# Optimization experiments

Measured on AMD Instinct MI355X. Metric: run time of the kernel, lower is better.

## Reference

```python
import jax, jax.numpy as jnp
import numpy as np

B, SW, SE, D, H, FF = 8, 512, 128, 1024, 16, 4096
HD = D // H
EPS = 1e-12
SCALE = 1.0 / np.sqrt(HD).astype(np.float32)


def _split_heads(x):
    # [B, S, D] -> [B, H, S, HD]
    b, s, _ = x.shape
    return x.reshape(b, s, H, HD).transpose(0, 2, 1, 3)


def _layer_norm(x, g, b):
    m = jnp.mean(x, axis=-1, keepdims=True)
    v = jnp.mean(jnp.square(x - m), axis=-1, keepdims=True)
    return g * (x - m) / jnp.sqrt(v + EPS) + b


def setup_inputs() -> dict:
    key = jax.random.key(0)
    ks = iter(jax.random.split(key, 40))
    std = 0.02

    def w(i, o):
        return jax.random.normal(next(ks), (i, o), jnp.float32) * std

    inp = {
        "word_hidden_states": jax.random.normal(next(ks), (B, SW, D), jnp.float32),
        "entity_hidden_states": jax.random.normal(next(ks), (B, SE, D), jnp.float32),
        "word_attention_mask": jnp.zeros((B, SW), jnp.float32),
        "entity_attention_mask": jnp.zeros((B, SE), jnp.float32),
        # entity-aware self attention projections
        "Wq": w(D, D), "bq": jnp.zeros((D,), jnp.float32),
        "Ww2e": w(D, D), "bw2e": jnp.zeros((D,), jnp.float32),
        "We2w": w(D, D), "be2w": jnp.zeros((D,), jnp.float32),
        "We2e": w(D, D), "be2e": jnp.zeros((D,), jnp.float32),
        "Wk": w(D, D), "bk": jnp.zeros((D,), jnp.float32),
        "Wv": w(D, D), "bv": jnp.zeros((D,), jnp.float32),
        # BertSelfOutput
        "Wo": w(D, D), "bo": jnp.zeros((D,), jnp.float32),
        "ln1_g": jnp.ones((D,), jnp.float32), "ln1_b": jnp.zeros((D,), jnp.float32),
        # BertIntermediate / BertOutput
        "Wi": w(D, FF), "bi": jnp.zeros((FF,), jnp.float32),
        "Wout": w(FF, D), "bout": jnp.zeros((D,), jnp.float32),
        "ln2_g": jnp.ones((D,), jnp.float32), "ln2_b": jnp.zeros((D,), jnp.float32),
    }
    return inp


def _layer(wh, eh, wmask, emask, Wq, bq, Ww2e, bw2e, We2w, be2w, We2e, be2e,
           Wk, bk, Wv, bv, Wo, bo, ln1_g, ln1_b, Wi, bi, Wout, bout, ln2_g, ln2_b):
    sw = wh.shape[1]
    hidden = jnp.concatenate([wh, eh], axis=1)              # [B, S, D]
    mask = jnp.concatenate([wmask, emask], axis=-1)[:, None, None, :]  # additive

    q_w2w = _split_heads(wh @ Wq + bq)
    q_w2e = _split_heads(wh @ Ww2e + bw2e)
    q_e2w = _split_heads(eh @ We2w + be2w)
    q_e2e = _split_heads(eh @ We2e + be2e)
    k = _split_heads(hidden @ Wk + bk)                      # [B, H, S, HD]
    kw, ke = k[:, :, :sw, :], k[:, :, sw:, :]

    s_w2w = jnp.einsum("bhqd,bhkd->bhqk", q_w2w, kw)
    s_w2e = jnp.einsum("bhqd,bhkd->bhqk", q_w2e, ke)
    s_e2w = jnp.einsum("bhqd,bhkd->bhqk", q_e2w, kw)
    s_e2e = jnp.einsum("bhqd,bhkd->bhqk", q_e2e, ke)
    word_scores = jnp.concatenate([s_w2w, s_w2e], axis=3)
    ent_scores = jnp.concatenate([s_e2w, s_e2e], axis=3)
    scores = jnp.concatenate([word_scores, ent_scores], axis=2) * SCALE + mask
    probs = jax.nn.softmax(scores, axis=-1)

    v = _split_heads(hidden @ Wv + bv)
    ctx = jnp.einsum("bhqk,bhkd->bhqd", probs, v)
    ctx = ctx.transpose(0, 2, 1, 3).reshape(wh.shape[0], -1, D)  # [B, S, D]

    # BertSelfOutput: dense + residual + LN
    attn_out = _layer_norm(ctx @ Wo + bo + hidden, ln1_g, ln1_b)
    # BertIntermediate + BertOutput
    inter = jax.nn.gelu(attn_out @ Wi + bi, approximate=False)
    out = _layer_norm(inter @ Wout + bout + attn_out, ln2_g, ln2_b)
    return out[:, :sw, :], out[:, sw:, :]


def reference(word_hidden_states, entity_hidden_states, word_attention_mask,
              entity_attention_mask, Wq, bq, Ww2e, bw2e, We2w, be2w, We2e, be2e,
              Wk, bk, Wv, bv, Wo, bo, ln1_g, ln1_b, Wi, bi, Wout, bout,
              ln2_g, ln2_b):
    return _layer(word_hidden_states, entity_hidden_states, word_attention_mask,
                  entity_attention_mask, Wq, bq, Ww2e, bw2e, We2w, be2w, We2e,
                  be2e, Wk, bk, Wv, bv, Wo, bo, ln1_g, ln1_b, Wi, bi, Wout,
                  bout, ln2_g, ln2_b)
```

## Files before the change

### kernel.cpp

```cpp
#include <hip/hip_runtime.h>
#include <hip/hip_bf16.h>
#include <stdint.h>
#include <math.h>

#define DEV __device__ __forceinline__

using bf16 = __hip_bfloat16;
typedef __attribute__((ext_vector_type(8))) short bf16x8;
typedef __attribute__((ext_vector_type(4))) float f32x4;

static constexpr int NB  = 8;
static constexpr int NSW = 512;
static constexpr int NSE = 128;
static constexpr int ND  = 1024;
static constexpr int NH  = 16;
static constexpr int NFF = 4096;
static constexpr int NS  = NSW + NSE;
static constexpr int NHD = 64;

DEV f32x4 mfma16(bf16x8 a, bf16x8 b, f32x4 c){
  return __builtin_amdgcn_mfma_f32_16x16x32_bf16(a, b, c, 0, 0, 0);
}

DEV void gload16(const bf16* g, bf16* l){
  __builtin_amdgcn_global_load_lds((const __attribute__((address_space(1))) void*)g,
                                   (__attribute__((address_space(3))) void*)l,
                                   16, 0, 0);
}

DEV bf16 tobf(float f){ return __float2bfloat16(f); }

union PK4 { bf16 h[4]; short4 s; };

__global__ __launch_bounds__(256) void cast_word_k(const float* __restrict__ wh,
                                                   bf16* __restrict__ hid){
  long i = ((long)blockIdx.x*256 + threadIdx.x)*4;
  float4 v = *reinterpret_cast<const float4*>(wh + i);
  PK4 p; p.h[0]=tobf(v.x); p.h[1]=tobf(v.y); p.h[2]=tobf(v.z); p.h[3]=tobf(v.w);
  long row = i >> 10; int c = (int)(i & 1023);
  int b = (int)(row >> 9), s = (int)(row & 511);
  *reinterpret_cast<short4*>(hid + ((long)(b*NS + s) << 10) + c) = p.s;
}

__global__ __launch_bounds__(256) void cast_ent_k(const float* __restrict__ eh,
                                                  bf16* __restrict__ hid){
  long i = ((long)blockIdx.x*256 + threadIdx.x)*4;
  float4 v = *reinterpret_cast<const float4*>(eh + i);
  PK4 p; p.h[0]=tobf(v.x); p.h[1]=tobf(v.y); p.h[2]=tobf(v.z); p.h[3]=tobf(v.w);
  long row = i >> 10; int c = (int)(i & 1023);
  int b = (int)(row >> 7), s = (int)(row & 127);
  *reinterpret_cast<short4*>(hid + ((long)(b*NS + NSW + s) << 10) + c) = p.s;
}

struct TP7 { const float* src[7]; bf16* dst[7]; };

__global__ void transpose7_k(TP7 tp){
  __shared__ float tile[32][33];
  const float* in = tp.src[blockIdx.z];
  bf16* out = tp.dst[blockIdx.z];
  const int c0 = blockIdx.x*32, r0 = blockIdx.y*32;
  const int tx = threadIdx.x, ty = threadIdx.y;
  #pragma unroll
  for (int i=0;i<4;i++)
    tile[ty + i*8][tx] = in[(long)(r0 + ty + i*8)*1024 + c0 + tx];
  __syncthreads();
  #pragma unroll
  for (int i=0;i<4;i++){
    int rr = ty + i*8;
    out[(long)(c0 + rr)*1024 + r0 + tx] = tobf(tile[tx][rr]);
  }
}

__global__ void transpose_cast_k(const float* __restrict__ in, bf16* __restrict__ out,
                                 int R, int C){
  __shared__ float tile[32][33];
  const int c0 = blockIdx.x*32, r0 = blockIdx.y*32;
  const int tx = threadIdx.x, ty = threadIdx.y;
  #pragma unroll
  for (int i=0;i<4;i++)
    tile[ty + i*8][tx] = in[(long)(r0 + ty + i*8)*C + c0 + tx];
  __syncthreads();
  #pragma unroll
  for (int i=0;i<4;i++){
    int rr = ty + i*8;
    out[(long)(c0 + rr)*R + r0 + tx] = tobf(tile[tx][rr]);
  }
}

__global__ void bias_concat_k(const float* __restrict__ bq, const float* __restrict__ bw2e,
                              const float* __restrict__ be2w, const float* __restrict__ be2e,
                              const float* __restrict__ bk, const float* __restrict__ bv,
                              float* __restrict__ bQw, float* __restrict__ bQe,
                              float* __restrict__ bKV){
  int i = blockIdx.x*256 + threadIdx.x;
  bQw[i] = bq[i];   bQw[1024+i] = bw2e[i];
  bQe[i] = be2w[i]; bQe[1024+i] = be2e[i];
  bKV[i] = bk[i];   bKV[1024+i] = bv[i];
}

template<int NF>
DEV void stage_issue(bf16* buf, const bf16* a0, const bf16* a1,
                     const bf16* b0, const bf16* b1, int koff, int tid){
  gload16(a0 + koff, buf + tid*8);
  gload16(a1 + koff, buf + (512 + tid)*8);
  gload16(b0 + koff, buf + (1024 + tid)*8);
  if constexpr (NF == 4) gload16(b1 + koff, buf + (1536 + tid)*8);
}

template<int NF>
DEV void g256_core(const bf16* a0, const bf16* a1,
                   const bf16* b0, const bf16* b1,
                   int NSs, bf16* lds, f32x4 (&acc)[8][NF],
                   int tid, int wr, int wc, int lane){
  constexpr int BUFE = (1024 + NF*256)*8;
  constexpr int LPS  = (NF == 4) ? 4 : 3;
  auto buf = [&](int s){ return lds + (s & 3)*BUFE; };

  stage_issue<NF>(buf(0), a0,a1,b0,b1, 0,  tid);
  stage_issue<NF>(buf(1), a0,a1,b0,b1, 32, tid);
  stage_issue<NF>(buf(2), a0,a1,b0,b1, 64, tid);

  for (int s=0; s<NSs; ++s){
    const int r = NSs - 1 - s;
    const int pend = (r >= 2 ? 2 : r) * LPS;
    if      (pend == 8) asm volatile("s_waitcnt vmcnt(8)" ::: "memory");
    else if (pend == 6) asm volatile("s_waitcnt vmcnt(6)" ::: "memory");
    else if (pend == 4) asm volatile("s_waitcnt vmcnt(4)" ::: "memory");
    else if (pend == 3) asm volatile("s_waitcnt vmcnt(3)" ::: "memory");
    else                asm volatile("s_waitcnt vmcnt(0)" ::: "memory");
    __builtin_amdgcn_sched_barrier(0);
    asm volatile("s_barrier" ::: "memory");
    __builtin_amdgcn_sched_barrier(0);

    if (s+3 < NSs) stage_issue<NF>(buf(s+3), a0,a1,b0,b1, (s+3)*32, tid);

    const bf16* Ar = buf(s);
    const bf16* Br = buf(s) + 1024*8;
    bf16x8 bfr[NF], afr[4];
    #pragma unroll
    for (int nf=0; nf<NF; ++nf)
      bfr[nf] = *reinterpret_cast<const bf16x8*>(Br + (((wc*NF+nf)<<6) + lane)*8);
    #pragma unroll
    for (int m=0; m<4; ++m)
      afr[m] = *reinterpret_cast<const bf16x8*>(Ar + (((wr*8+m)<<6) + lane)*8);
    __builtin_amdgcn_s_setprio(1);
    #pragma unroll
    for (int m=0; m<4; ++m)
      #pragma unroll
      for (int nf=0; nf<NF; ++nf)
        acc[m][nf] = mfma16(afr[m], bfr[nf], acc[m][nf]);
    __builtin_amdgcn_s_setprio(0);
    #pragma unroll
    for (int m=0; m<4; ++m)
      afr[m] = *reinterpret_cast<const bf16x8*>(Ar + (((wr*8+4+m)<<6) + lane)*8);
    __builtin_amdgcn_s_setprio(1);
    #pragma unroll
    for (int m=0; m<4; ++m)
      #pragma unroll
      for (int nf=0; nf<NF; ++nf)
        acc[4+m][nf] = mfma16(afr[m], bfr[nf], acc[4+m][nf]);
    __builtin_amdgcn_s_setprio(0);
  }
}

__global__ __launch_bounds__(512, 2) void proj_k(const bf16* __restrict__ hid,
    const bf16* __restrict__ WqwT, const bf16* __restrict__ WqeT,
    const bf16* __restrict__ WkvT,
    const float* __restrict__ bQw, const float* __restrict__ bQe,
    const float* __restrict__ bKV,
    bf16* __restrict__ Qwb, bf16* __restrict__ Qeb,
    bf16* __restrict__ KVb, bf16* __restrict__ Vt){
  __shared__ __align__(16) bf16 lds[4*16384];
  const int tid = threadIdx.x, wid = tid>>6, lane = tid&63;
  const int wr = wid>>2, wc = wid&3, lr = lane&15, lg = lane>>4;
  int wg = blockIdx.x;
  { int xcd = wg & 7, idx = wg >> 3; wg = xcd*40 + idx; }
  const bool isKV = (wg >= 160);
  const int loc = isKV ? wg - 160 : wg;
  const int m0 = (loc >> 3)*256, n0 = (loc & 7)*256;
  const bool word = (m0 < 4096);

  const int la = lane & 15, ksub = (lane>>4)*8;
  auto hidrow = [&](int r)->long{
    if (isKV) return r;
    if (word) return (long)((r>>9)*640 + (r&511));
    int r2 = r - 4096; return (long)((r2>>7)*640 + 512 + (r2&127));
  };
  const bf16* a0 = hid + hidrow(m0 + wid*16 + la)*1024 + ksub;
  const bf16* a1 = hid + hidrow(m0 + (wid+8)*16 + la)*1024 + ksub;
  const bf16* Bt = isKV ? WkvT : (word ? WqwT : WqeT);
  const bf16* b0 = Bt + (long)(n0 + wid*16 + la)*1024 + ksub;
  const bf16* b1 = Bt + (long)(n0 + (wid+8)*16 + la)*1024 + ksub;

  f32x4 acc[8][4];
  #pragma unroll
  for (int m=0;m<8;m++)
    #pragma unroll
    for (int n=0;n<4;n++) acc[m][n] = (f32x4){0.f,0.f,0.f,0.f};

  g256_core<4>(a0, a1, b0, b1, 32, lds, acc, tid, wr, wc, lane);

  const float* bias = isKV ? bKV : (word ? bQw : bQe);
  #pragma unroll
  for (int m=0;m<8;m++){
    const int rbase = m0 + wr*128 + m*16 + lg*4;
    #pragma unroll
    for (int nf=0;nf<4;nf++){
      const int col = n0 + wc*64 + nf*16 + lr;
      const float bsv = bias[col];
      #pragma unroll
      for (int r=0;r<4;r++){
        const int rw = rbase + r;
        const float v = acc[m][nf][r] + bsv;
        if (!isKV){
          if (word) Qwb[(long)rw*2048 + col] = tobf(v);
          else      Qeb[(long)(rw-4096)*2048 + col] = tobf(v);
        } else {
          if (col < 1024){
            KVb[(long)rw*2048 + col] = tobf(v);
          } else {
            int b = rw / NS, s = rw % NS, hh = (col-1024)>>6, dd = (col-1024)&63;
            Vt[((long)((b*NH + hh)*NHD + dd))*NS + s] = tobf(v);
          }
        }
      }
    }
  }
}

__global__ __launch_bounds__(512, 2) void ffn1_k(const bf16* __restrict__ A,
    const bf16* __restrict__ Bt, const float* __restrict__ bias,
    bf16* __restrict__ out){
  __shared__ __align__(16) bf16 lds[4*16384];
  const int tid = threadIdx.x, wid = tid>>6, lane = tid&63;
  const int wr = wid>>2, wc = wid&3, lr = lane&15, lg = lane>>4;
  int wg = blockIdx.x;
  { int xcd = wg & 7, idx = wg >> 3; wg = xcd*40 + idx; }
  const int m0 = (wg >> 4)*256, n0 = (wg & 15)*256;

  const int la = lane & 15, ksub = (lane>>4)*8;
  const bf16* a0 = A + (long)(m0 + wid*16 + la)*1024 + ksub;
  const bf16* a1 = A + (long)(m0 + (wid+8)*16 + la)*1024 + ksub;
  const bf16* b0 = Bt + (long)(n0 + wid*16 + la)*1024 + ksub;
  const bf16* b1 = Bt + (long)(n0 + (wid+8)*16 + la)*1024 + ksub;

  f32x4 acc[8][4];
  #pragma unroll
  for (int m=0;m<8;m++)
    #pragma unroll
    for (int n=0;n<4;n++) acc[m][n] = (f32x4){0.f,0.f,0.f,0.f};

  g256_core<4>(a0, a1, b0, b1, 32, lds, acc, tid, wr, wc, lane);

  #pragma unroll
  for (int m=0;m<8;m++){
    const int rbase = m0 + wr*128 + m*16 + lg*4;
    #pragma unroll
    for (int nf=0;nf<4;nf++){
      const int col = n0 + wc*64 + nf*16 + lr;
      const float bsv = bias[col];
      #pragma unroll
      for (int r=0;r<4;r++){
        float v = acc[m][nf][r] + bsv;
        float ge = 0.5f*v*(1.0f + erff(v*0.70710678118654752f));
        out[(long)(rbase+r)*NFF + col] = tobf(ge);
      }
    }
  }
}

__global__ __launch_bounds__(512, 2) void ws_k(const bf16* __restrict__ A, int lda,
    const bf16* __restrict__ Bt, const float* __restrict__ bias,
    float* __restrict__ out0, float* __restrict__ out1, int Kc){
  __shared__ __align__(16) bf16 lds[4*12288];
  const int tid = threadIdx.x, wid = tid>>6, lane = tid&63;
  const int wr = wid>>2, wc = wid&3, lr = lane&15, lg = lane>>4;
  int wg = blockIdx.x;
  { int xcd = wg & 7, idx = wg >> 3; wg = xcd*20 + idx; }
  const int m0 = (wg >> 3)*256, n0 = (wg & 7)*128;
  const int kt0 = blockIdx.z * Kc;

  const int la = lane & 15, ksub = (lane>>4)*8;
  const bf16* a0 = A + (long)(m0 + wid*16 + la)*lda + kt0 + ksub;
  const bf16* a1 = A + (long)(m0 + (wid+8)*16 + la)*lda + kt0 + ksub;
  const bf16* b0 = Bt + (long)(n0 + wid*16 + la)*lda + kt0 + ksub;

  f32x4 acc[8][2];
  #pragma unroll
  for (int m=0;m<8;m++)
    #pragma unroll
    for (int n=0;n<2;n++) acc[m][n] = (f32x4){0.f,0.f,0.f,0.f};

  g256_core<2>(a0, a1, b0, b0, Kc/32, lds, acc, tid, wr, wc, lane);

  float* out = blockIdx.z ? out1 : out0;
  #pragma unroll
  for (int m=0;m<8;m++){
    const int rbase = m0 + wr*128 + m*16 + lg*4;
    #pragma unroll
    for (int nf=0;nf<2;nf++){
      const int col = n0 + wc*32 + nf*16 + lr;
      const float bsv = blockIdx.z ? 0.f : bias[col];
      #pragma unroll
      for (int r=0;r<4;r++)
        out[(long)(rbase+r)*1024 + col] = acc[m][nf][r] + bsv;
    }
  }
}

__global__ __launch_bounds__(256) void attn_k(
    const bf16* __restrict__ Qw, const bf16* __restrict__ Qe,
    const bf16* __restrict__ KV, const bf16* __restrict__ Vt,
    const float* __restrict__ wm, const float* __restrict__ em,
    bf16* __restrict__ ctx){
  __shared__ __align__(16) bf16 Plds[4][2][16*40];
  __shared__ float mred[4][2][16];
  __shared__ float lred[4][2][16];
  __shared__ __align__(16) float accred[4][16][64];
  const int tid = threadIdx.x, wid = tid>>6, lane = tid&63;
  const int lr = lane&15, lg = lane>>4;
  const int w   = blockIdx.x;
  const int b   = w / (NH*20);
  const int rem = w % (NH*20);
  const int h   = rem / 20;
  const int q0  = (rem % 20)*32;

  const bf16* Qbase; long qrow0;
  if (q0 < NSW){ Qbase = Qw; qrow0 = (long)b*NSW + q0; }
  else         { Qbase = Qe; qrow0 = (long)b*NSE + (q0 - NSW); }

  bf16x8 qA[2][2], qB[2][2];
  #pragma unroll
  for (int m=0;m<2;m++)
    #pragma unroll
    for (int dc=0; dc<2; dc++){
      long o = (qrow0 + m*16 + lr)*2048 + h*NHD + dc*32 + lg*8;
      qA[m][dc] = *reinterpret_cast<const bf16x8*>(Qbase + o);
      qB[m][dc] = *reinterpret_cast<const bf16x8*>(Qbase + o + 1024);
    }

  const f32x4 zero = {0.f,0.f,0.f,0.f};
  f32x4 cacc[2][4];
  float mrow[2][4], lsum[2][4];
  #pragma unroll
  for (int m=0;m<2;m++){
    #pragma unroll
    for (int dt=0;dt<4;dt++) cacc[m][dt] = zero;
    #pragma unroll
    for (int r=0;r<4;r++){ mrow[m][r] = -1e30f; lsum[m][r] = 0.f; }
  }

  const bf16* Kbase = KV + (long)b*NS*2048 + h*NHD;
  const bf16* Vbase = Vt + (long)((b*NH + h)*NHD)*NS;

  for (int kt=wid*5; kt<wid*5+5; kt++){
    const int k0 = kt*32;
    const bool word = (k0 < NSW);

    bf16x8 kf[2][2], vf[4];
    #pragma unroll
    for (int sub=0;sub<2;sub++)
      #pragma unroll
      for (int dc=0;dc<2;dc++)
        kf[sub][dc] = *reinterpret_cast<const bf16x8*>(
            Kbase + (long)(k0 + sub*16 + lr)*2048 + dc*32 + lg*8);
    #pragma unroll
    for (int dt=0;dt<4;dt++)
      vf[dt] = *reinterpret_cast<const bf16x8*>(
          Vbase + (long)(dt*16 + lr)*NS + k0 + lg*8);

    float msk0, msk1;
    { int k = k0 + lr;
      msk0 = word ? wm[b*NSW + k]      : em[b*NSE + (k - NSW)];
      msk1 = word ? wm[b*NSW + k + 16] : em[b*NSE + (k + 16 - NSW)];
    }

    f32x4 sc[2][2];
    #pragma unroll
    for (int m=0;m<2;m++){ sc[m][0]=zero; sc[m][1]=zero; }
    __builtin_amdgcn_s_setprio(1);
    #pragma unroll
    for (int m=0;m<2;m++)
      #pragma unroll
      for (int sub=0;sub<2;sub++)
        #pragma unroll
        for (int dc=0;dc<2;dc++){
          const bf16x8 q = word ? qA[m][dc] : qB[m][dc];
          sc[m][sub] = mfma16(q, kf[sub][dc], sc[m][sub]);
        }
    __builtin_amdgcn_s_setprio(0);

    #pragma unroll
    for (int m=0;m<2;m++){
      bf16* pw = &Plds[wid][m][0];
      #pragma unroll
      for (int r=0;r<4;r++){
        float s0 = sc[m][0][r]*0.125f + msk0;
        float s1 = sc[m][1][r]*0.125f + msk1;
        float t = fmaxf(s0, s1);
        #pragma unroll
        for (int o=8;o;o>>=1) t = fmaxf(t, __shfl_xor(t, o, 16));
        float mn = fmaxf(mrow[m][r], t);
        float al = __expf(mrow[m][r] - mn);
        mrow[m][r] = mn;
        float p0 = __expf(s0 - mn), p1 = __expf(s1 - mn);
        float ps = p0 + p1;
        #pragma unroll
        for (int o=8;o;o>>=1) ps += __shfl_xor(ps, o, 16);
        lsum[m][r] = lsum[m][r]*al + ps;
        pw[(lg*4+r)*40 + lr]      = tobf(p0);
        pw[(lg*4+r)*40 + 16 + lr] = tobf(p1);
        #pragma unroll
        for (int dt=0;dt<4;dt++) cacc[m][dt][r] *= al;
      }
    }

    __builtin_amdgcn_s_setprio(1);
    #pragma unroll
    for (int m=0;m<2;m++){
      bf16x8 pa = *reinterpret_cast<const bf16x8*>(&Plds[wid][m][0] + lr*40 + lg*8);
      #pragma unroll
      for (int dt=0;dt<4;dt++)
        cacc[m][dt] = mfma16(pa, vf[dt], cacc[m][dt]);
    }
    __builtin_amdgcn_s_setprio(0);
  }

  #pragma unroll
  for (int m=0;m<2;m++)
    #pragma unroll
    for (int r=0;r<4;r++)
      if (lr == 0){
        mred[wid][m][lg*4+r] = mrow[m][r];
        lred[wid][m][lg*4+r] = lsum[m][r];
      }
  __syncthreads();

  float Lg[2][4], scl[2][4];
  #pragma unroll
  for (int m=0;m<2;m++)
    #pragma unroll
    for (int r=0;r<4;r++){
      const int row = lg*4 + r;
      float M0 = fmaxf(fmaxf(mred[0][m][row], mred[1][m][row]),
                       fmaxf(mred[2][m][row], mred[3][m][row]));
      float lt = 0.f;
      #pragma unroll
      for (int ww=0; ww<4; ww++)
        lt += lred[ww][m][row] * __expf(mred[ww][m][row] - M0);
      Lg[m][r]  = lt;
      scl[m][r] = __expf(mrow[m][r] - M0);
    }

  const long crow = (long)b*NS + q0;
  #pragma unroll
  for (int m=0;m<2;m++){
    #pragma unroll
    for (int dt=0;dt<4;dt++)
      #pragma unroll
      for (int r=0;r<4;r++)
        accred[wid][dt*4+r][lane] = cacc[m][dt][r] * scl[m][r];
    __syncthreads();
    { const int dt = wid;
      #pragma unroll
      for (int r=0;r<4;r++){
        float s = accred[0][dt*4+r][lane] + accred[1][dt*4+r][lane]
                + accred[2][dt*4+r][lane] + accred[3][dt*4+r][lane];
        s /= Lg[m][r];
        ctx[(crow + m*16 + lg*4 + r)*ND + h*NHD + dt*16 + lr] = tobf(s);
      }
    }
    __syncthreads();
  }
}

DEV void block_red2(float& s1, float& s2){
  __shared__ float red[8];
  #pragma unroll
  for (int o=32;o;o>>=1){ s1 += __shfl_down(s1,o); s2 += __shfl_down(s2,o); }
  int wid = threadIdx.x>>6, lane = threadIdx.x&63;
  if (lane==0){ red[wid]=s1; red[4+wid]=s2; }
  __syncthreads();
  s1 = red[0]+red[1]+red[2]+red[3];
  s2 = red[4]+red[5]+red[6]+red[7];
}

__global__ __launch_bounds__(256) void ln1_k(const float* __restrict__ ctxO,
    const float* __restrict__ ctxO1,
    const float* __restrict__ wh, const float* __restrict__ eh,
    const float* __restrict__ g, const float* __restrict__ be,
    float* __restrict__ outF, bf16* __restrict__ outB){
  const int row = blockIdx.x;
  const int b = row / NS, s = row % NS;
  const float* resid = (s < NSW) ? wh + ((long)(b*NSW + s))*ND
                                 : eh + ((long)(b*NSE + (s-NSW)))*ND;
  const int t = threadIdx.x;
  float4 xv = reinterpret_cast<const float4*>(ctxO + (long)row*ND)[t];
  float4 x1 = reinterpret_cast<const float4*>(ctxO1 + (long)row*ND)[t];
  float4 rv = reinterpret_cast<const float4*>(resid)[t];
  float4 x = make_float4(xv.x+x1.x+rv.x, xv.y+x1.y+rv.y, xv.z+x1.z+rv.z, xv.w+x1.w+rv.w);
  float s1 = x.x+x.y+x.z+x.w;
  float s2 = x.x*x.x + x.y*x.y + x.z*x.z + x.w*x.w;
  block_red2(s1, s2);
  float mean = s1 * (1.f/ND);
  float var  = s2 * (1.f/ND) - mean*mean;
  float rstd = rsqrtf(var + 1e-12f);
  float4 gv = reinterpret_cast<const float4*>(g)[t];
  float4 bv = reinterpret_cast<const float4*>(be)[t];
  float4 y = make_float4(gv.x*(x.x-mean)*rstd + bv.x,
                         gv.y*(x.y-mean)*rstd + bv.y,
                         gv.z*(x.z-mean)*rstd + bv.z,
                         gv.w*(x.w-mean)*rstd + bv.w);
  reinterpret_cast<float4*>(outF + (long)row*ND)[t] = y;
  PK4 p; p.h[0]=tobf(y.x); p.h[1]=tobf(y.y); p.h[2]=tobf(y.z); p.h[3]=tobf(y.w);
  reinterpret_cast<short4*>(outB + (long)row*ND)[t] = p.s;
}

__global__ __launch_bounds__(256) void ln2_k(const float* __restrict__ ffo,
    const float* __restrict__ ffo1,
    const float* __restrict__ attnF, const float* __restrict__ g,
    const float* __restrict__ be, float* __restrict__ out){
  const int row = blockIdx.x;
  const int b = row / NS, s = row % NS;
  const int t = threadIdx.x;
  float4 xv = reinterpret_cast<const float4*>(ffo + (long)row*ND)[t];
  float4 x1 = reinterpret_cast<const float4*>(ffo1 + (long)row*ND)[t];
  float4 rv = reinterpret_cast<const float4*>(attnF + (long)row*ND)[t];
  float4 x = make_float4(xv.x+x1.x+rv.x, xv.y+x1.y+rv.y, xv.z+x1.z+rv.z, xv.w+x1.w+rv.w);
  float s1 = x.x+x.y+x.z+x.w;
  float s2 = x.x*x.x + x.y*x.y + x.z*x.z + x.w*x.w;
  block_red2(s1, s2);
  float mean = s1 * (1.f/ND);
  float var  = s2 * (1.f/ND) - mean*mean;
  float rstd = rsqrtf(var + 1e-12f);
  float4 gv = reinterpret_cast<const float4*>(g)[t];
  float4 bv = reinterpret_cast<const float4*>(be)[t];
  float4 y = make_float4(gv.x*(x.x-mean)*rstd + bv.x,
                         gv.y*(x.y-mean)*rstd + bv.y,
                         gv.z*(x.z-mean)*rstd + bv.z,
                         gv.w*(x.w-mean)*rstd + bv.w);
  float* op = (s < NSW) ? out + ((long)(b*NSW+s))*ND
                        : out + (long)NB*NSW*ND + ((long)(b*NSE + (s-NSW)))*ND;
  reinterpret_cast<float4*>(op)[t] = y;
}

extern "C" void kernel_launch(void* const* d_in, const int* in_sizes, int n_in,
                              void* d_out, int out_size, void* d_ws, size_t ws_size,
                              hipStream_t stream){
  (void)in_sizes; (void)n_in; (void)out_size; (void)ws_size;
  const float* wh   = (const float*)d_in[0];
  const float* eh   = (const float*)d_in[1];
  const float* wm   = (const float*)d_in[2];
  const float* em   = (const float*)d_in[3];
  const float* Wq   = (const float*)d_in[4];   const float* bq   = (const float*)d_in[5];
  const float* Ww2e = (const float*)d_in[6];   const float* bw2e = (const float*)d_in[7];
  const float* We2w = (const float*)d_in[8];   const float* be2w = (const float*)d_in[9];
  const float* We2e = (const float*)d_in[10];  const float* be2e = (const float*)d_in[11];
  const float* Wk   = (const float*)d_in[12];  const float* bk   = (const float*)d_in[13];
  const float* Wv   = (const float*)d_in[14];  const float* bv   = (const float*)d_in[15];
  const float* Wo   = (const float*)d_in[16];  const float* bo   = (const float*)d_in[17];
  const float* g1   = (const float*)d_in[18];  const float* b1   = (const float*)d_in[19];
  const float* Wi   = (const float*)d_in[20];  const float* bi   = (const float*)d_in[21];
  const float* Wout = (const float*)d_in[22];  const float* bout = (const float*)d_in[23];
  const float* g2   = (const float*)d_in[24];  const float* b2   = (const float*)d_in[25];
  float* out = (float*)d_out;

  char* ws = (char*)d_ws;
  size_t off = 0;
  auto alloc = [&](size_t bytes)->char*{
    char* p = ws + off; off += (bytes + 255) & ~(size_t)255; return p;
  };

  bf16* hid   = (bf16*)alloc((size_t)NB*NS*ND*2);
  bf16* WqwT  = (bf16*)alloc((size_t)2048*ND*2);
  bf16* WqeT  = (bf16*)alloc((size_t)2048*ND*2);
  bf16* WkvT  = (bf16*)alloc((size_t)2048*ND*2);
  float* part1 = (float*)hid;
  bf16* WoT   = (bf16*)alloc((size_t)ND*ND*2);
  bf16* WiT   = (bf16*)alloc((size_t)NFF*ND*2);
  bf16* WoutT = (bf16*)alloc((size_t)ND*NFF*2);
  float* bQw  = (float*)alloc(2048*4);
  float* bQe  = (float*)alloc(2048*4);
  float* bKV  = (float*)alloc(2048*4);

  char* u1 = alloc((size_t)52428800);
  bf16* Qwb = (bf16*)u1;
  bf16* Qeb = Qwb + (size_t)NB*NSW*2048;
  bf16* KVb = Qeb + (size_t)NB*NSE*2048;
  bf16* Vt  = KVb + (size_t)NB*NS*2048;
  bf16* inter = (bf16*)u1;
  bf16* attnB = (bf16*)(u1 + (size_t)41943040);

  bf16*  ctx   = (bf16*)alloc((size_t)NB*NS*ND*2);
  float* ctxO  = (float*)alloc((size_t)NB*NS*ND*4);
  float* ffo   = ctxO;
  float* attnF = (float*)alloc((size_t)NB*NS*ND*4);

  dim3 tb(32,8);
  cast_word_k<<<4096, 256, 0, stream>>>(wh, hid);
  cast_ent_k <<<1024, 256, 0, stream>>>(eh, hid);

  TP7 tp;
  tp.src[0]=Wq;   tp.dst[0]=WqwT;
  tp.src[1]=Ww2e; tp.dst[1]=WqwT + (size_t)1024*1024;
  tp.src[2]=We2w; tp.dst[2]=WqeT;
  tp.src[3]=We2e; tp.dst[3]=WqeT + (size_t)1024*1024;
  tp.src[4]=Wk;   tp.dst[4]=WkvT;
  tp.src[5]=Wv;   tp.dst[5]=WkvT + (size_t)1024*1024;
  tp.src[6]=Wo;   tp.dst[6]=WoT;
  transpose7_k<<<dim3(32,32,7), tb, 0, stream>>>(tp);
  transpose_cast_k<<<dim3(128,32), tb, 0, stream>>>(Wi,   WiT,   ND, NFF);
  transpose_cast_k<<<dim3(32,128), tb, 0, stream>>>(Wout, WoutT, NFF, ND);
  bias_concat_k<<<4, 256, 0, stream>>>(bq, bw2e, be2w, be2e, bk, bv, bQw, bQe, bKV);

  proj_k<<<320, 512, 0, stream>>>(hid, WqwT, WqeT, WkvT, bQw, bQe, bKV,
                                  Qwb, Qeb, KVb, Vt);

  attn_k<<<2560, 256, 0, stream>>>(Qwb, Qeb, KVb, Vt, wm, em, ctx);

  ws_k<<<dim3(160,1,2), 512, 0, stream>>>(ctx, 1024, WoT, bo, ctxO, part1, 512);
  ln1_k<<<5120, 256, 0, stream>>>(ctxO, part1, wh, eh, g1, b1, attnF, attnB);
  ffn1_k<<<320, 512, 0, stream>>>(attnB, WiT, bi, inter);
  ws_k<<<dim3(160,1,2), 512, 0, stream>>>(inter, 4096, WoutT, bout, ffo, part1, 2048);
  ln2_k<<<5120, 256, 0, stream>>>(ffo, part1, attnF, g2, b2, out);
}
```

Baseline: 635.9 us.

## Replace 4-stage LDS ring with double-buffered LDS and register fragment ping-pong

Swaps the 4-deep LDS ring buffer with 3 stages in flight for a 2-buffer LDS scheme. All A/B fragments for the next stage are read into registers before the MFMAs of the current stage run, so LDS reads overlap with matrix math. LDS per block is halved, which may help occupancy. In exchange only one global prefetch is in flight, each gate waits on vmcnt(0) and lgkmcnt(0), and holding two full fragment sets raises register pressure.

After: 697.6 us. +9.7%, slower.

```diff
diff --git a/kernel.cpp b/kernel.cpp
--- a/kernel.cpp
+++ b/kernel.cpp
@@ -108,58 +108,64 @@
 }
 
 template<int NF>
+struct Frags { bf16x8 a[8]; bf16x8 b[NF]; };
+
+template<int NF>
+DEV void read_frags(const bf16* bufp, Frags<NF>& f, int wr, int wc, int lane){
+  #pragma unroll
+  for (int nf=0; nf<NF; ++nf)
+    f.b[nf] = *reinterpret_cast<const bf16x8*>(bufp + 1024*8 + (((wc*NF+nf)<<6)+lane)*8);
+  #pragma unroll
+  for (int m=0; m<8; ++m)
+    f.a[m] = *reinterpret_cast<const bf16x8*>(bufp + (((wr*8+m)<<6)+lane)*8);
+}
+
+template<int NF>
+DEV void do_mfma(const Frags<NF>& f, f32x4 (&acc)[8][NF]){
+  __builtin_amdgcn_s_setprio(1);
+  #pragma unroll
+  for (int m=0; m<8; ++m)
+    #pragma unroll
+    for (int nf=0; nf<NF; ++nf)
+      acc[m][nf] = mfma16(f.a[m], f.b[nf], acc[m][nf]);
+  __builtin_amdgcn_s_setprio(0);
+}
+
+#define G256_GATE() do{ \
+  asm volatile("s_waitcnt vmcnt(0) lgkmcnt(0)" ::: "memory"); \
+  __builtin_amdgcn_sched_barrier(0); \
+  asm volatile("s_barrier" ::: "memory"); \
+  __builtin_amdgcn_sched_barrier(0); }while(0)
+
+template<int NF>
 DEV void g256_core(const bf16* a0, const bf16* a1,
                    const bf16* b0, const bf16* b1,
                    int NSs, bf16* lds, f32x4 (&acc)[8][NF],
                    int tid, int wr, int wc, int lane){
   constexpr int BUFE = (1024 + NF*256)*8;
-  constexpr int LPS  = (NF == 4) ? 4 : 3;
-  auto buf = [&](int s){ return lds + (s & 3)*BUFE; };
-
-  stage_issue<NF>(buf(0), a0,a1,b0,b1, 0,  tid);
-  stage_issue<NF>(buf(1), a0,a1,b0,b1, 32, tid);
-  stage_issue<NF>(buf(2), a0,a1,b0,b1, 64, tid);
-
-  for (int s=0; s<NSs; ++s){
-    const int r = NSs - 1 - s;
-    const int pend = (r >= 2 ? 2 : r) * LPS;
-    if      (pend == 8) asm volatile("s_waitcnt vmcnt(8)" ::: "memory");
-    else if (pend == 6) asm volatile("s_waitcnt vmcnt(6)" ::: "memory");
-    else if (pend == 4) asm volatile("s_waitcnt vmcnt(4)" ::: "memory");
-    else if (pend == 3) asm volatile("s_waitcnt vmcnt(3)" ::: "memory");
-    else                asm volatile("s_waitcnt vmcnt(0)" ::: "memory");
-    __builtin_amdgcn_sched_barrier(0);
-    asm volatile("s_barrier" ::: "memory");
-    __builtin_amdgcn_sched_barrier(0);
-
-    if (s+3 < NSs) stage_issue<NF>(buf(s+3), a0,a1,b0,b1, (s+3)*32, tid);
-
-    const bf16* Ar = buf(s);
-    const bf16* Br = buf(s) + 1024*8;
-    bf16x8 bfr[NF], afr[4];
-    #pragma unroll
-    for (int nf=0; nf<NF; ++nf)
-      bfr[nf] = *reinterpret_cast<const bf16x8*>(Br + (((wc*NF+nf)<<6) + lane)*8);
-    #pragma unroll
-    for (int m=0; m<4; ++m)
-      afr[m] = *reinterpret_cast<const bf16x8*>(Ar + (((wr*8+m)<<6) + lane)*8);
-    __builtin_amdgcn_s_setprio(1);
-    #pragma unroll
-    for (int m=0; m<4; ++m)
-      #pragma unroll
-      for (int nf=0; nf<NF; ++nf)
-        acc[m][nf] = mfma16(afr[m], bfr[nf], acc[m][nf]);
-    __builtin_amdgcn_s_setprio(0);
-    #pragma unroll
-    for (int m=0; m<4; ++m)
-      afr[m] = *reinterpret_cast<const bf16x8*>(Ar + (((wr*8+4+m)<<6) + lane)*8);
-    __builtin_amdgcn_s_setprio(1);
-    #pragma unroll
-    for (int m=0; m<4; ++m)
-      #pragma unroll
-      for (int nf=0; nf<NF; ++nf)
-        acc[4+m][nf] = mfma16(afr[m], bfr[nf], acc[4+m][nf]);
-    __builtin_amdgcn_s_setprio(0);
+  bf16* s0p = lds;
+  bf16* s1p = lds + BUFE;
+  Frags<NF> fA, fB;
+
+  stage_issue<NF>(s0p, a0,a1,b0,b1, 0, tid);
+  asm volatile("s_waitcnt vmcnt(0)" ::: "memory");
+  __builtin_amdgcn_sched_barrier(0);
+  asm volatile("s_barrier" ::: "memory");
+  __builtin_amdgcn_sched_barrier(0);
+  stage_issue<NF>(s1p, a0,a1,b0,b1, 32, tid);
+  read_frags<NF>(s0p, fA, wr, wc, lane);
+
+  for (int s=0; s<NSs; s+=2){
+    G256_GATE();
+    if (s+2 < NSs) stage_issue<NF>(s0p, a0,a1,b0,b1, (s+2)*32, tid);
+    read_frags<NF>(s1p, fB, wr, wc, lane);
+    do_mfma<NF>(fA, acc);
+    if (s+2 < NSs){
+      G256_GATE();
+      if (s+3 < NSs) stage_issue<NF>(s1p, a0,a1,b0,b1, (s+3)*32, tid);
+      read_frags<NF>(s0p, fA, wr, wc, lane);
+    }
+    do_mfma<NF>(fB, acc);
   }
 }
 
@@ -170,7 +176,7 @@
     const float* __restrict__ bKV,
     bf16* __restrict__ Qwb, bf16* __restrict__ Qeb,
     bf16* __restrict__ KVb, bf16* __restrict__ Vt){
-  __shared__ __align__(16) bf16 lds[4*16384];
+  __shared__ __align__(16) bf16 lds[2*16384];
   const int tid = threadIdx.x, wid = tid>>6, lane = tid&63;
   const int wr = wid>>2, wc = wid&3, lr = lane&15, lg = lane>>4;
   int wg = blockIdx.x;
@@ -231,7 +237,7 @@
 __global__ __launch_bounds__(512, 2) void ffn1_k(const bf16* __restrict__ A,
     const bf16* __restrict__ Bt, const float* __restrict__ bias,
     bf16* __restrict__ out){
-  __shared__ __align__(16) bf16 lds[4*16384];
+  __shared__ __align__(16) bf16 lds[2*16384];
   const int tid = threadIdx.x, wid = tid>>6, lane = tid&63;
   const int wr = wid>>2, wc = wid&3, lr = lane&15, lg = lane>>4;
   int wg = blockIdx.x;
@@ -272,7 +278,7 @@
 __global__ __launch_bounds__(512, 2) void ws_k(const bf16* __restrict__ A, int lda,
     const bf16* __restrict__ Bt, const float* __restrict__ bias,
     float* __restrict__ out0, float* __restrict__ out1, int Kc){
-  __shared__ __align__(16) bf16 lds[4*12288];
+  __shared__ __align__(16) bf16 lds[2*12288];
   const int tid = threadIdx.x, wid = tid>>6, lane = tid&63;
   const int wr = wid>>2, wc = wid&3, lr = lane&15, lg = lane>>4;
   int wg = blockIdx.x;
```
